# Optimization experiments

Measured on AMD Instinct MI355X. Metric: run time of the kernel, lower is better.

The kernel has to match this reference:

```python
import jax, jax.numpy as jnp
import numpy as np

B, N, C = 64, 196, 768
H = 12
HD = C // H            # 64
TOPK = int(0.25 * HD)  # 16
HIDDEN = int(C * 4.0)  # 3072
SCALE = HD ** -0.5
EPS = 1e-5


def layernorm(x, g, b):
    mu = jnp.mean(x, axis=-1, keepdims=True)
    var = jnp.var(x, axis=-1, keepdims=True)
    return (x - mu) * jax.lax.rsqrt(var + EPS) * g + b


def setup_inputs() -> dict:
    key = jax.random.key(0)
    ks = jax.random.split(key, 8)
    s = 0.02
    return {
        "x": jax.random.normal(ks[0], (B, N, C), jnp.float32),
        "norm1_g": jnp.ones((C,), jnp.float32),
        "norm1_b": jnp.zeros((C,), jnp.float32),
        "qk_w": jax.random.normal(ks[1], (2 * C, C), jnp.float32) * s,   # torch Linear [out,in], no bias
        "attn_proj_w": jax.random.normal(ks[2], (C, H * TOPK), jnp.float32) * s,
        "attn_proj_b": jnp.zeros((C,), jnp.float32),
        "norm2_g": jnp.ones((C,), jnp.float32),
        "norm2_b": jnp.zeros((C,), jnp.float32),
        "fc1_w": jax.random.normal(ks[3], (HIDDEN, C), jnp.float32) * s,
        "fc1_b": jnp.zeros((HIDDEN,), jnp.float32),
        "fc2_w": jax.random.normal(ks[4], (C, HIDDEN), jnp.float32) * s,
        "fc2_b": jnp.zeros((C,), jnp.float32),
    }


def reference(x, norm1_g, norm1_b, qk_w, attn_proj_w, attn_proj_b,
              norm2_g, norm2_b, fc1_w, fc1_b, fc2_w, fc2_b):
    # --- HomoAttention branch ---
    h = layernorm(x, norm1_g, norm1_b)                       # [B,N,C]
    qk = h @ qk_w.T                                          # [B,N,2C]
    qk = qk.reshape(B, N, 2, H, HD).transpose(2, 0, 3, 1, 4) # [2,B,H,N,HD]
    q, k = qk[0] * SCALE, qk[1]
    attn = jnp.einsum('bhnd,bhmd->bhnm', q, k)               # [B,H,N,N]
    top_vals, _ = jax.lax.top_k(attn, TOPK)                  # [B,H,N,TOPK]
    a = jax.nn.softmax(top_vals, axis=-1)
    a = a.transpose(0, 2, 1, 3).reshape(B, N, H * TOPK)      # [B,N,H*TOPK]
    x = x + a @ attn_proj_w.T + attn_proj_b

    # --- MLP branch ---
    h2 = layernorm(x, norm2_g, norm2_b)
    h2 = jax.nn.gelu(h2 @ fc1_w.T + fc1_b, approximate=False)
    x = x + h2 @ fc2_w.T + fc2_b
    return x
```

## Files before the change

kernel.cpp:

```cpp
#include <hip/hip_runtime.h>


#define BATCH 64
#define SEQ   196
#define CH    768
#define NHEAD 12
#define HDIM  64
#define TOPK  16
#define HID   3072
#define MROWS 12544
#define MHALF 6272
#define SCALE_F 0.125f
#define NEGBIG -3e38f

typedef __bf16 bf16x8 __attribute__((ext_vector_type(8)));
typedef float  f32x4  __attribute__((ext_vector_type(4)));

__device__ __forceinline__ unsigned short f2b(float f) {
    union { float f; unsigned int i; } c; c.f = f;
    unsigned int u = c.i;
    return (unsigned short)((u + 0x7fffu + ((u >> 16) & 1u)) >> 16);
}
__device__ __forceinline__ float b2f(unsigned short u) {
    union { unsigned int i; float f; } c; c.i = ((unsigned int)u) << 16; return c.f;
}

__device__ __forceinline__ float gelu_f(float v) {
    float u = v * (0.7978845608f + 0.0356774081f * v * v);
    float e = __expf(2.0f * u);
    float th = 1.0f - 2.0f / (e + 1.0f);
    return 0.5f * v * (1.0f + th);
}

__device__ __forceinline__ void async16(const unsigned short* g, unsigned short* l) {
    __builtin_amdgcn_global_load_lds(
        (const __attribute__((address_space(1))) unsigned int*)(g),
        (__attribute__((address_space(3))) unsigned int*)(l), 16, 0, 0);
}

__global__ __launch_bounds__(256) void f2b4_k(const float* __restrict__ s0, unsigned short* __restrict__ d0, int n0,
                                              const float* __restrict__ s1, unsigned short* __restrict__ d1, int n1,
                                              const float* __restrict__ s2, unsigned short* __restrict__ d2, int n2,
                                              const float* __restrict__ s3, unsigned short* __restrict__ d3, int n3)
{
    int idx = (blockIdx.x * 256 + threadIdx.x) * 4;
    const float* s; unsigned short* d; int n;
    if (idx < n0) { s = s0; d = d0; n = n0; }
    else {
        idx -= n0;
        if (idx < n1) { s = s1; d = d1; n = n1; }
        else {
            idx -= n1;
            if (idx < n2) { s = s2; d = d2; n = n2; }
            else { idx -= n2; s = s3; d = d3; n = n3; }
        }
    }
    if (idx < n) {
        float4 v = *(const float4*)(s + idx);
        ushort4 o;
        o.x = f2b(v.x); o.y = f2b(v.y); o.z = f2b(v.z); o.w = f2b(v.w);
        *(ushort4*)(d + idx) = o;
    }
}

template<bool INF32>
__global__ __launch_bounds__(256) void ln_k(const void* __restrict__ xin,
                                            const float* __restrict__ gw,
                                            const float* __restrict__ bw,
                                            unsigned short* __restrict__ out)
{
    const int row = blockIdx.x;
    const int tid = threadIdx.x;
    float v0, v1, v2;
    if constexpr (INF32) {
        const float* xr = (const float*)xin + (size_t)row * CH;
        v0 = xr[tid]; v1 = xr[tid + 256]; v2 = xr[tid + 512];
    } else {
        const unsigned short* xr = (const unsigned short*)xin + (size_t)row * CH;
        v0 = b2f(xr[tid]); v1 = b2f(xr[tid + 256]); v2 = b2f(xr[tid + 512]);
    }
    float s  = v0 + v1 + v2;
    float sq = v0*v0 + v1*v1 + v2*v2;
#pragma unroll
    for (int off = 32; off > 0; off >>= 1) {
        s  += __shfl_down(s, off, 64);
        sq += __shfl_down(sq, off, 64);
    }
    __shared__ __align__(16) float red[8];
    if ((tid & 63) == 0) { red[(tid >> 6) * 2] = s; red[(tid >> 6) * 2 + 1] = sq; }
    __syncthreads();
    s  = red[0] + red[2] + red[4] + red[6];
    sq = red[1] + red[3] + red[5] + red[7];
    float mu  = s * (1.0f / CH);
    float var = sq * (1.0f / CH) - mu * mu;
    float rs  = rsqrtf(var + 1e-5f);
    unsigned short* orow = out + (size_t)row * CH;
    orow[tid]       = f2b((v0 - mu) * rs * gw[tid]       + bw[tid]);
    orow[tid + 256] = f2b((v1 - mu) * rs * gw[tid + 256] + bw[tid + 256]);
    orow[tid + 512] = f2b((v2 - mu) * rs * gw[tid + 512] + bw[tid + 512]);
}

template<int TM, int TN, bool BIAS, int RES, bool GELU, bool OUTF>
__global__ __launch_bounds__(256, 4)
void gemm_bt(const unsigned short* __restrict__ A,
             const unsigned short* __restrict__ Bw,
             const float* __restrict__ bias,
             const void* __restrict__ resid,
             void* __restrict__ Cout,
             int M, int N, int K)
{
    constexpr int WROWS = (TM == 128) ? 2 : 1;
    constexpr int WCOLS = 4 / WROWS;
    constexpr int JF = TN / (16 * WCOLS);
    __shared__ __align__(16) unsigned short As[2][TM * 32];
    __shared__ __align__(16) unsigned short Bs[2][TN * 32];
    const int tid  = threadIdx.x;
    const int w    = tid >> 6;
    const int lane = tid & 63;

    const int gridN = gridDim.x, gridM = gridDim.y;
    const int lid = blockIdx.y * gridN + blockIdx.x;
    const int SG = 8 * gridN;
    const int sg = lid / SG, r = lid % SG;
    const int remM = gridM - sg * 8;
    int mloc, nloc;
    if (remM >= 8) { mloc = sg * 8 + (r & 7); nloc = r >> 3; }
    else           { mloc = sg * 8 + r % remM; nloc = r / remM; }
    const int tileM = mloc * TM;
    const int tileN = nloc * TN;

    const int wm = (w / WCOLS) * 64;
    const int wn = (w % WCOLS) * (JF * 16);
    const int q   = lane >> 4;
    const int l16 = lane & 15;
    const int csw = (q ^ (l16 & 3)) * 8;

    f32x4 acc[4][JF];
#pragma unroll
    for (int i = 0; i < 4; ++i)
#pragma unroll
        for (int j = 0; j < JF; ++j) acc[i][j] = (f32x4){0.f, 0.f, 0.f, 0.f};

    const int r0 = tid >> 2;
    const int g0 = ((tid & 3) ^ (r0 & 3)) * 8;

    const unsigned short* pB[TN / 64];
    const unsigned short* pA[TM / 64];
#pragma unroll
    for (int c = 0; c < TN / 64; ++c) pB[c] = Bw + (size_t)(tileN + r0 + c * 64) * K + g0;
#pragma unroll
    for (int c = 0; c < TM / 64; ++c) pA[c] = A + (size_t)(tileM + r0 + c * 64) * K + g0;

    auto stage = [&](int buf) {
#pragma unroll
        for (int c = 0; c < TN / 64; ++c) {
            async16(pB[c], &Bs[buf][(size_t)(c * 256 + w * 64) * 8]);
            pB[c] += 32;
        }
#pragma unroll
        for (int c = 0; c < TM / 64; ++c) {
            async16(pA[c], &As[buf][(size_t)(c * 256 + w * 64) * 8]);
            pA[c] += 32;
        }
    };

    const int kIters = K >> 5;
    stage(0);
    int cur = 0;
    for (int kt = 0; kt < kIters; ++kt) {
        __syncthreads();
        if (kt + 1 < kIters) stage(cur ^ 1);
        bf16x8 af[4], bfr[JF];
#pragma unroll
        for (int i = 0; i < 4; ++i)
            af[i] = *(const bf16x8*)&As[cur][(wm + i * 16 + l16) * 32 + csw];
#pragma unroll
        for (int j = 0; j < JF; ++j)
            bfr[j] = *(const bf16x8*)&Bs[cur][(wn + j * 16 + l16) * 32 + csw];
#pragma unroll
        for (int i = 0; i < 4; ++i)
#pragma unroll
            for (int j = 0; j < JF; ++j)
                acc[i][j] = __builtin_amdgcn_mfma_f32_16x16x32_bf16(af[i], bfr[j], acc[i][j], 0, 0, 0);
        cur ^= 1;
    }

#pragma unroll
    for (int i = 0; i < 4; ++i) {
#pragma unroll
        for (int r2 = 0; r2 < 4; ++r2) {
            int row = tileM + wm + i * 16 + q * 4 + r2;
#pragma unroll
            for (int j = 0; j < JF; ++j) {
                int col = tileN + wn + j * 16 + l16;
                float v = acc[i][j][r2];
                if (BIAS) v += bias[col];
                if (GELU) v = gelu_f(v);
                if (RES == 1) v += ((const float*)resid)[(size_t)row * N + col];
                if (RES == 2) v += b2f(((const unsigned short*)resid)[(size_t)row * N + col]);
                if (OUTF) ((float*)Cout)[(size_t)row * N + col] = v;
                else      ((unsigned short*)Cout)[(size_t)row * N + col] = f2b(v);
            }
        }
    }
}

template<int KC, bool BIAS, int RES, bool GELU, bool OUTF>
__global__ __launch_bounds__(512, 2)
void gemm8p(const unsigned short* __restrict__ A,
            const unsigned short* __restrict__ Bw,
            const float* __restrict__ bias,
            const void* __restrict__ resid,
            void* __restrict__ Cout,
            int M, int N)
{
    constexpr int T = KC / 64;
    __shared__ __align__(16) unsigned short As[2][256 * 64];
    __shared__ __align__(16) unsigned short Bs[2][256 * 64];
    const int tid  = threadIdx.x;
    const int w    = tid >> 6;
    const int lane = tid & 63;
    const int q    = lane >> 4;
    const int l16  = lane & 15;

    const int gridN = gridDim.x, gridM = gridDim.y;
    const int lid = blockIdx.y * gridN + blockIdx.x;
    const int SG = 8 * gridN;
    const int sg = lid / SG, rr = lid % SG;
    const int remM = gridM - sg * 8;
    int mloc, nloc;
    if (remM >= 8) { mloc = sg * 8 + (rr & 7); nloc = rr >> 3; }
    else           { mloc = sg * 8 + rr % remM; nloc = rr / remM; }
    const int tileM = mloc * 256, tileN = nloc * 256;

    const int wm = (w >> 2) * 128;
    const int wn = (w & 3) * 64;

    const int r0 = tid >> 3;
    const int g0 = (tid & 7) ^ (r0 & 7);
    const int rB = r0 + (r0 & 32);
    const unsigned short* pAsrc = A  + (size_t)(tileM + r0) * KC + g0 * 8;
    const unsigned short* pBsrc = Bw + (size_t)(tileN + rB) * KC + g0 * 8;

    auto stageA = [&](int v, int j) {
        const unsigned short* s = pAsrc + (size_t)(j * 64) * KC + v * 64;
        unsigned short* d = As[v & 1] + j * 4096 + w * 512;
        async16(s, d);
        async16(s + (size_t)128 * KC, d + 8192);
    };
    auto stageB = [&](int v, int j) {
        const unsigned short* s = pBsrc + (size_t)(j * 32) * KC + v * 64;
        unsigned short* d = Bs[v & 1] + j * 2048 + (w * 8 + ((w & 4) << 3)) * 64;
        async16(s, d);
        async16(s + (size_t)128 * KC, d + 8192);
    };

    f32x4 acc[8][4];
#pragma unroll
    for (int i = 0; i < 8; ++i)
#pragma unroll
        for (int jn = 0; jn < 4; ++jn) acc[i][jn] = (f32x4){0.f, 0.f, 0.f, 0.f};

    stageA(0, 0); stageB(0, 0); stageB(0, 1); stageA(0, 1);
    asm volatile("s_waitcnt vmcnt(4)" ::: "memory");
    __builtin_amdgcn_s_barrier();
    asm volatile("" ::: "memory");

    const int arow = wm + l16;
    const int brow = wn + l16;
    const int xsw  = l16 & 7;

#pragma unroll 2
    for (int u = 0; u < T; ++u) {
        const unsigned short* Ab = As[u & 1];
        const unsigned short* Bb = Bs[u & 1];
        bf16x8 af[4][2], b0[2][2], b1[2][2];

#pragma unroll
        for (int m = 0; m < 4; ++m)
#pragma unroll
            for (int kk = 0; kk < 2; ++kk)
                af[m][kk] = *(const bf16x8*)&Ab[(arow + m * 16) * 64 + ((((kk << 2) | q) ^ xsw) << 3)];
#pragma unroll
        for (int n = 0; n < 2; ++n)
#pragma unroll
            for (int kk = 0; kk < 2; ++kk)
                b0[n][kk] = *(const bf16x8*)&Bb[(brow + n * 16) * 64 + ((((kk << 2) | q) ^ xsw) << 3)];
        if (u + 1 < T) stageA(u + 1, 0);
        __builtin_amdgcn_s_setprio(1);
#pragma unroll
        for (int kk = 0; kk < 2; ++kk)
#pragma unroll
            for (int m = 0; m < 4; ++m)
#pragma unroll
                for (int n = 0; n < 2; ++n)
                    acc[m][n] = __builtin_amdgcn_mfma_f32_16x16x32_bf16(af[m][kk], b0[n][kk], acc[m][n], 0, 0, 0);
        __builtin_amdgcn_s_setprio(0);

        if (u + 1 < T) asm volatile("s_waitcnt vmcnt(4)" ::: "memory");
        else           asm volatile("s_waitcnt vmcnt(2)" ::: "memory");
        __builtin_amdgcn_s_barrier();
        asm volatile("" ::: "memory");
#pragma unroll
        for (int n = 0; n < 2; ++n)
#pragma unroll
            for (int kk = 0; kk < 2; ++kk)
                b1[n][kk] = *(const bf16x8*)&Bb[(brow + 32 + n * 16) * 64 + ((((kk << 2) | q) ^ xsw) << 3)];
        if (u + 1 < T) stageB(u + 1, 0);
        __builtin_amdgcn_s_setprio(1);
#pragma unroll
        for (int kk = 0; kk < 2; ++kk)
#pragma unroll
            for (int m = 0; m < 4; ++m)
#pragma unroll
                for (int n = 0; n < 2; ++n)
                    acc[m][2 + n] = __builtin_amdgcn_mfma_f32_16x16x32_bf16(af[m][kk], b1[n][kk], acc[m][2 + n], 0, 0, 0);
        __builtin_amdgcn_s_setprio(0);

        if (u + 1 < T) asm volatile("s_waitcnt vmcnt(4)" ::: "memory");
        else           asm volatile("s_waitcnt vmcnt(0)" ::: "memory");
        __builtin_amdgcn_s_barrier();
        asm volatile("" ::: "memory");
#pragma unroll
        for (int m = 0; m < 4; ++m)
#pragma unroll
            for (int kk = 0; kk < 2; ++kk)
                af[m][kk] = *(const bf16x8*)&Ab[(arow + 64 + m * 16) * 64 + ((((kk << 2) | q) ^ xsw) << 3)];
        if (u + 1 < T) stageB(u + 1, 1);
        __builtin_amdgcn_s_setprio(1);
#pragma unroll
        for (int kk = 0; kk < 2; ++kk)
#pragma unroll
            for (int m = 0; m < 4; ++m)
#pragma unroll
                for (int n = 0; n < 2; ++n)
                    acc[4 + m][2 + n] = __builtin_amdgcn_mfma_f32_16x16x32_bf16(af[m][kk], b1[n][kk], acc[4 + m][2 + n], 0, 0, 0);
        __builtin_amdgcn_s_setprio(0);

        if (u + 1 < T) {
            stageA(u + 1, 1);
            asm volatile("s_waitcnt vmcnt(4)" ::: "memory");
            __builtin_amdgcn_s_barrier();
            asm volatile("" ::: "memory");
        }
        __builtin_amdgcn_s_setprio(1);
#pragma unroll
        for (int kk = 0; kk < 2; ++kk)
#pragma unroll
            for (int m = 0; m < 4; ++m)
#pragma unroll
                for (int n = 0; n < 2; ++n)
                    acc[4 + m][n] = __builtin_amdgcn_mfma_f32_16x16x32_bf16(af[m][kk], b0[n][kk], acc[4 + m][n], 0, 0, 0);
        __builtin_amdgcn_s_setprio(0);
    }

#pragma unroll
    for (int mh = 0; mh < 2; ++mh)
#pragma unroll
        for (int m = 0; m < 4; ++m)
#pragma unroll
            for (int r2 = 0; r2 < 4; ++r2) {
                const int row = tileM + wm + mh * 64 + m * 16 + q * 4 + r2;
#pragma unroll
                for (int nh = 0; nh < 2; ++nh)
#pragma unroll
                    for (int n = 0; n < 2; ++n) {
                        const int col = tileN + wn + nh * 32 + n * 16 + l16;
                        float v = acc[mh * 4 + m][nh * 2 + n][r2];
                        if (BIAS) v += bias[col];
                        if (GELU) v = gelu_f(v);
                        if (RES == 1) v += ((const float*)resid)[(size_t)row * N + col];
                        if (RES == 2) v += b2f(((const unsigned short*)resid)[(size_t)row * N + col]);
                        if (OUTF) ((float*)Cout)[(size_t)row * N + col] = v;
                        else      ((unsigned short*)Cout)[(size_t)row * N + col] = f2b(v);
                    }
            }
    (void)M;
}

__global__ __launch_bounds__(256) void attn_topk(const unsigned short* __restrict__ qk,
                                                 unsigned short* __restrict__ aout)
{
    const int bh = blockIdx.x;
    const int b = bh / NHEAD, h = bh % NHEAD;
    __shared__ __align__(16) unsigned short Qs[208 * 64];
    __shared__ __align__(16) unsigned short Ks[208 * 64];
    const int tid = threadIdx.x;

    for (int i = tid; i < 208 * 8; i += 256) {
        int row = i >> 3, c = i & 7;
        uint4 vq = make_uint4(0, 0, 0, 0), vk = vq;
        if (row < SEQ) {
            const uint4* gp = (const uint4*)(qk + ((size_t)(b * SEQ + row) * 1536 + h * 64));
            vq = gp[c];
            vk = gp[c + 96];
        }
        int slot = c ^ (row & 7);
        *(uint4*)&Qs[row * 64 + slot * 8] = vq;
        *(uint4*)&Ks[row * 64 + slot * 8] = vk;
    }
    __syncthreads();

    const int w = tid >> 6, lane = tid & 63;
    const int q = lane >> 4, l16 = lane & 15;

    for (int tn = w; tn < 13; tn += 4) {
        const int nrow = tn * 16 + l16;
        const int nsw = nrow & 7;
        bf16x8 bq0 = *(const bf16x8*)&Qs[nrow * 64 + ((0 * 4 + q) ^ nsw) * 8];
        bf16x8 bq1 = *(const bf16x8*)&Qs[nrow * 64 + ((1 * 4 + q) ^ nsw) * 8];

        float t[TOPK];
#pragma unroll
        for (int j = 0; j < TOPK; ++j) t[j] = NEGBIG;

        for (int tm = 0; tm < 12; ++tm) {
            const int mrow = tm * 16 + l16;
            const int msw = mrow & 7;
            bf16x8 ak0 = *(const bf16x8*)&Ks[mrow * 64 + ((0 * 4 + q) ^ msw) * 8];
            bf16x8 ak1 = *(const bf16x8*)&Ks[mrow * 64 + ((1 * 4 + q) ^ msw) * 8];
            f32x4 acc = (f32x4){0.f, 0.f, 0.f, 0.f};
            acc = __builtin_amdgcn_mfma_f32_16x16x32_bf16(ak0, bq0, acc, 0, 0, 0);
            acc = __builtin_amdgcn_mfma_f32_16x16x32_bf16(ak1, bq1, acc, 0, 0, 0);
#pragma unroll
            for (int r = 0; r < 4; ++r) {
                float v = acc[r];
#pragma unroll
                for (int j = 0; j < TOPK; ++j) {
                    float mx = fmaxf(t[j], v);
                    v = fminf(t[j], v);
                    t[j] = mx;
                }
            }
        }
        {
            const int mrow = 12 * 16 + l16;
            const int msw = mrow & 7;
            bf16x8 ak0 = *(const bf16x8*)&Ks[mrow * 64 + ((0 * 4 + q) ^ msw) * 8];
            bf16x8 ak1 = *(const bf16x8*)&Ks[mrow * 64 + ((1 * 4 + q) ^ msw) * 8];
            f32x4 acc = (f32x4){0.f, 0.f, 0.f, 0.f};
            acc = __builtin_amdgcn_mfma_f32_16x16x32_bf16(ak0, bq0, acc, 0, 0, 0);
            acc = __builtin_amdgcn_mfma_f32_16x16x32_bf16(ak1, bq1, acc, 0, 0, 0);
#pragma unroll
            for (int r = 0; r < 4; ++r) {
                float v = (q == 0) ? acc[r] : NEGBIG;
#pragma unroll
                for (int j = 0; j < TOPK; ++j) {
                    float mx = fmaxf(t[j], v);
                    v = fminf(t[j], v);
                    t[j] = mx;
                }
            }
        }

#pragma unroll
        for (int stage = 0; stage < 2; ++stage) {
            const int xm = 16 << stage;
            float bl[TOPK], c[TOPK];
#pragma unroll
            for (int j = 0; j < TOPK; ++j) bl[j] = __shfl_xor(t[j], xm, 64);
#pragma unroll
            for (int j = 0; j < TOPK; ++j) c[j] = fmaxf(t[j], bl[TOPK - 1 - j]);
#pragma unroll
            for (int s = 8; s >= 1; s >>= 1) {
#pragma unroll
                for (int i = 0; i < TOPK; ++i) {
                    if ((i & s) == 0) {
                        float mx = fmaxf(c[i], c[i + s]);
                        c[i + s] = fminf(c[i], c[i + s]);
                        c[i] = mx;
                    }
                }
            }
#pragma unroll
            for (int j = 0; j < TOPK; ++j) t[j] = c[j];
        }

        if (q == 0 && nrow < SEQ) {
            float e[TOPK], sum = 0.f;
#pragma unroll
            for (int j = 0; j < TOPK; ++j) { e[j] = __expf((t[j] - t[0]) * SCALE_F); sum += e[j]; }
            float inv = 1.0f / sum;
            unsigned int pk[8];
#pragma unroll
            for (int jj = 0; jj < 8; ++jj)
                pk[jj] = (unsigned int)f2b(e[2 * jj] * inv) |
                         ((unsigned int)f2b(e[2 * jj + 1] * inv) << 16);
            unsigned short* dst = aout + ((size_t)(b * SEQ + nrow)) * (NHEAD * TOPK) + h * TOPK;
            ((uint4*)dst)[0] = make_uint4(pk[0], pk[1], pk[2], pk[3]);
            ((uint4*)dst)[1] = make_uint4(pk[4], pk[5], pk[6], pk[7]);
        }
    }
}

extern "C" void kernel_launch(void* const* d_in, const int* in_sizes, int n_in,
                              void* d_out, int out_size, void* d_ws, size_t ws_size,
                              hipStream_t stream)
{
    const float* x    = (const float*)d_in[0];
    const float* g1   = (const float*)d_in[1];
    const float* bb1  = (const float*)d_in[2];
    const float* qkw  = (const float*)d_in[3];
    const float* pw   = (const float*)d_in[4];
    const float* pb   = (const float*)d_in[5];
    const float* g2   = (const float*)d_in[6];
    const float* bb2  = (const float*)d_in[7];
    const float* f1w  = (const float*)d_in[8];
    const float* f1b  = (const float*)d_in[9];
    const float* f2w  = (const float*)d_in[10];
    const float* f2bp = (const float*)d_in[11];
    float* out = (float*)d_out;

    char* ws = (char*)d_ws;
    const size_t SZ_H   = (size_t)MROWS * CH * 2;
    const size_t N_WQK  = (size_t)2 * CH * CH;
    const size_t N_WP   = (size_t)CH * (NHEAD * TOPK);
    const size_t N_WF   = (size_t)HID * CH;
    const size_t SZ_W   = (N_WQK + N_WP + 2 * N_WF) * 2;
    const size_t SZ_A   = (size_t)MROWS * (NHEAD * TOPK) * 2;
    const size_t SZ_QK  = (size_t)MROWS * 2 * CH * 2;
    const size_t SZ_GGF = (size_t)MROWS * HID * 2;

    unsigned short* hbuf = (unsigned short*)(ws);
    unsigned short* wqk  = (unsigned short*)(ws + SZ_H);
    unsigned short* wp   = wqk + N_WQK;
    unsigned short* wf1  = wp  + N_WP;
    unsigned short* wf2  = wf1 + N_WF;
    unsigned short* av   = (unsigned short*)(ws + SZ_H + SZ_W);
    unsigned short* qk   = (unsigned short*)(ws + SZ_H + SZ_W + SZ_A);
    unsigned short* gg   = qk;

    const size_t base = SZ_H + SZ_W + SZ_A;
    const bool fullMLP = ws_size >= base + SZ_GGF + SZ_H;
    const bool bx1     = fullMLP || ws_size >= base + SZ_QK + SZ_H;
    unsigned short* x1b = (unsigned short*)(ws + base + (fullMLP ? SZ_GGF : SZ_QK));
    float* x1 = out;

    {
        int total4 = (int)((N_WQK + N_WP + 2 * N_WF) / 4);
        f2b4_k<<<(total4 + 255) / 256, 256, 0, stream>>>(
            qkw, wqk, (int)N_WQK, pw, wp, (int)N_WP,
            f1w, wf1, (int)N_WF, f2w, wf2, (int)N_WF);
    }

    ln_k<true><<<MROWS, 256, 0, stream>>>(x, g1, bb1, hbuf);
    gemm8p<CH, false, 0, false, false><<<dim3(2 * CH / 256, MROWS / 256), 512, 0, stream>>>(
        hbuf, wqk, nullptr, nullptr, qk, MROWS, 2 * CH);
    attn_topk<<<BATCH * NHEAD, 256, 0, stream>>>(qk, av);

    if (bx1) {
        gemm_bt<64, 128, true, 1, false, false><<<dim3(6, 196), 256, 0, stream>>>(
            av, wp, pb, x, x1b, MROWS, CH, NHEAD * TOPK);
        ln_k<false><<<MROWS, 256, 0, stream>>>(x1b, g2, bb2, hbuf);
        if (fullMLP) {
            gemm8p<CH, true, 0, true, false><<<dim3(HID / 256, MROWS / 256), 512, 0, stream>>>(
                hbuf, wf1, f1b, nullptr, gg, MROWS, HID);
            gemm8p<HID, true, 2, false, true><<<dim3(CH / 256, MROWS / 256), 512, 0, stream>>>(
                gg, wf2, f2bp, x1b, out, MROWS, CH);
        } else {
            for (int half = 0; half < 2; ++half) {
                const size_t ro = (size_t)half * MHALF;
                gemm_bt<128, 128, true, 0, true, false><<<dim3(24, 49), 256, 0, stream>>>(
                    hbuf + ro * CH, wf1, f1b, nullptr, gg, MHALF, HID, CH);
                gemm_bt<64, 256, true, 2, false, true><<<dim3(3, 98), 256, 0, stream>>>(
                    gg, wf2, f2bp, x1b + ro * CH, out + ro * CH, MHALF, CH, HID);
            }
        }
    } else {
        gemm_bt<64, 128, true, 1, false, true><<<dim3(6, 196), 256, 0, stream>>>(
            av, wp, pb, x, x1, MROWS, CH, NHEAD * TOPK);
        ln_k<true><<<MROWS, 256, 0, stream>>>(x1, g2, bb2, hbuf);
        for (int half = 0; half < 2; ++half) {
            const size_t ro = (size_t)half * MHALF;
            gemm_bt<128, 128, true, 0, true, false><<<dim3(24, 49), 256, 0, stream>>>(
                hbuf + ro * CH, wf1, f1b, nullptr, gg, MHALF, HID, CH);
            gemm_bt<64, 256, true, 1, false, true><<<dim3(3, 98), 256, 0, stream>>>(
                gg, wf2, f2bp, x1 + ro * CH, out + ro * CH, MHALF, CH, HID);
        }
    }
}
```

Before: 436.8 us.

## Make gemm8p persistent with cross-tile prefetch and LDS-staged vectorized epilogue

```diff
diff --git a/kernel.cpp b/kernel.cpp
--- a/kernel.cpp
+++ b/kernel.cpp
@@ -215,6 +215,7 @@
             int M, int N)
 {
     constexpr int T = KC / 64;
+    static_assert((T & 1) == 0, "T must be even for persistent parity");
     __shared__ __align__(16) unsigned short As[2][256 * 64];
     __shared__ __align__(16) unsigned short Bs[2][256 * 64];
     const int tid  = threadIdx.x;
@@ -223,15 +224,19 @@
     const int q    = lane >> 4;
     const int l16  = lane & 15;
 
-    const int gridN = gridDim.x, gridM = gridDim.y;
-    const int lid = blockIdx.y * gridN + blockIdx.x;
-    const int SG = 8 * gridN;
-    const int sg = lid / SG, rr = lid % SG;
-    const int remM = gridM - sg * 8;
-    int mloc, nloc;
-    if (remM >= 8) { mloc = sg * 8 + (rr & 7); nloc = rr >> 3; }
-    else           { mloc = sg * 8 + rr % remM; nloc = rr / remM; }
-    const int tileM = mloc * 256, tileN = nloc * 256;
+    const int gridN = N >> 8, gridM = M >> 8;
+    const int nt = gridN * gridM;
+    const int P = gridDim.x;
+
+    auto tileOf = [&](int lid2, int& tm, int& tn) {
+        const int SG = 8 * gridN;
+        const int sg = lid2 / SG, rr2 = lid2 % SG;
+        const int remM = gridM - sg * 8;
+        int mloc, nloc;
+        if (remM >= 8) { mloc = sg * 8 + (rr2 & 7); nloc = rr2 >> 3; }
+        else           { mloc = sg * 8 + rr2 % remM; nloc = rr2 / remM; }
+        tm = mloc * 256; tn = nloc * 256;
+    };
 
     const int wm = (w >> 2) * 128;
     const int wn = (w & 3) * 64;
@@ -239,143 +244,229 @@
     const int r0 = tid >> 3;
     const int g0 = (tid & 7) ^ (r0 & 7);
     const int rB = r0 + (r0 & 32);
-    const unsigned short* pAsrc = A  + (size_t)(tileM + r0) * KC + g0 * 8;
-    const unsigned short* pBsrc = Bw + (size_t)(tileN + rB) * KC + g0 * 8;
-
-    auto stageA = [&](int v, int j) {
-        const unsigned short* s = pAsrc + (size_t)(j * 64) * KC + v * 64;
-        unsigned short* d = As[v & 1] + j * 4096 + w * 512;
-        async16(s, d);
-        async16(s + (size_t)128 * KC, d + 8192);
-    };
-    auto stageB = [&](int v, int j) {
-        const unsigned short* s = pBsrc + (size_t)(j * 32) * KC + v * 64;
-        unsigned short* d = Bs[v & 1] + j * 2048 + (w * 8 + ((w & 4) << 3)) * 64;
-        async16(s, d);
-        async16(s + (size_t)128 * KC, d + 8192);
-    };
-
-    f32x4 acc[8][4];
-#pragma unroll
-    for (int i = 0; i < 8; ++i)
-#pragma unroll
-        for (int jn = 0; jn < 4; ++jn) acc[i][jn] = (f32x4){0.f, 0.f, 0.f, 0.f};
-
-    stageA(0, 0); stageB(0, 0); stageB(0, 1); stageA(0, 1);
-    asm volatile("s_waitcnt vmcnt(4)" ::: "memory");
-    __builtin_amdgcn_s_barrier();
-    asm volatile("" ::: "memory");
 
     const int arow = wm + l16;
     const int brow = wn + l16;
     const int xsw  = l16 & 7;
 
-#pragma unroll 2
-    for (int u = 0; u < T; ++u) {
-        const unsigned short* Ab = As[u & 1];
-        const unsigned short* Bb = Bs[u & 1];
-        bf16x8 af[4][2], b0[2][2], b1[2][2];
-
-#pragma unroll
-        for (int m = 0; m < 4; ++m)
-#pragma unroll
-            for (int kk = 0; kk < 2; ++kk)
-                af[m][kk] = *(const bf16x8*)&Ab[(arow + m * 16) * 64 + ((((kk << 2) | q) ^ xsw) << 3)];
-#pragma unroll
-        for (int n = 0; n < 2; ++n)
-#pragma unroll
-            for (int kk = 0; kk < 2; ++kk)
-                b0[n][kk] = *(const bf16x8*)&Bb[(brow + n * 16) * 64 + ((((kk << 2) | q) ^ xsw) << 3)];
-        if (u + 1 < T) stageA(u + 1, 0);
-        __builtin_amdgcn_s_setprio(1);
-#pragma unroll
-        for (int kk = 0; kk < 2; ++kk)
-#pragma unroll
-            for (int m = 0; m < 4; ++m)
-#pragma unroll
-                for (int n = 0; n < 2; ++n)
-                    acc[m][n] = __builtin_amdgcn_mfma_f32_16x16x32_bf16(af[m][kk], b0[n][kk], acc[m][n], 0, 0, 0);
-        __builtin_amdgcn_s_setprio(0);
-
-        if (u + 1 < T) asm volatile("s_waitcnt vmcnt(4)" ::: "memory");
-        else           asm volatile("s_waitcnt vmcnt(2)" ::: "memory");
-        __builtin_amdgcn_s_barrier();
-        asm volatile("" ::: "memory");
-#pragma unroll
-        for (int n = 0; n < 2; ++n)
-#pragma unroll
-            for (int kk = 0; kk < 2; ++kk)
-                b1[n][kk] = *(const bf16x8*)&Bb[(brow + 32 + n * 16) * 64 + ((((kk << 2) | q) ^ xsw) << 3)];
-        if (u + 1 < T) stageB(u + 1, 0);
-        __builtin_amdgcn_s_setprio(1);
-#pragma unroll
-        for (int kk = 0; kk < 2; ++kk)
-#pragma unroll
-            for (int m = 0; m < 4; ++m)
-#pragma unroll
-                for (int n = 0; n < 2; ++n)
-                    acc[m][2 + n] = __builtin_amdgcn_mfma_f32_16x16x32_bf16(af[m][kk], b1[n][kk], acc[m][2 + n], 0, 0, 0);
-        __builtin_amdgcn_s_setprio(0);
-
-        if (u + 1 < T) asm volatile("s_waitcnt vmcnt(4)" ::: "memory");
-        else           asm volatile("s_waitcnt vmcnt(0)" ::: "memory");
-        __builtin_amdgcn_s_barrier();
-        asm volatile("" ::: "memory");
-#pragma unroll
-        for (int m = 0; m < 4; ++m)
-#pragma unroll
-            for (int kk = 0; kk < 2; ++kk)
-                af[m][kk] = *(const bf16x8*)&Ab[(arow + 64 + m * 16) * 64 + ((((kk << 2) | q) ^ xsw) << 3)];
-        if (u + 1 < T) stageB(u + 1, 1);
-        __builtin_amdgcn_s_setprio(1);
-#pragma unroll
-        for (int kk = 0; kk < 2; ++kk)
-#pragma unroll
-            for (int m = 0; m < 4; ++m)
-#pragma unroll
-                for (int n = 0; n < 2; ++n)
-                    acc[4 + m][2 + n] = __builtin_amdgcn_mfma_f32_16x16x32_bf16(af[m][kk], b1[n][kk], acc[4 + m][2 + n], 0, 0, 0);
-        __builtin_amdgcn_s_setprio(0);
-
-        if (u + 1 < T) {
-            stageA(u + 1, 1);
+    for (int t = (int)blockIdx.x; t < nt; t += P) {
+        int tileM, tileN;
+        tileOf(t, tileM, tileN);
+        const bool hasNext = (t + P) < nt;
+        int tileM2 = tileM, tileN2 = tileN;
+        if (hasNext) tileOf(t + P, tileM2, tileN2);
+
+        const unsigned short* pA0  = A  + (size_t)(tileM  + r0) * KC + g0 * 8;
+        const unsigned short* pB0  = Bw + (size_t)(tileN  + rB) * KC + g0 * 8;
+        const unsigned short* pA0n = A  + (size_t)(tileM2 + r0) * KC + g0 * 8;
+        const unsigned short* pB0n = Bw + (size_t)(tileN2 + rB) * KC + g0 * 8;
+
+        auto stageA = [&](int v, int j) {
+            const unsigned short* base = (v == T) ? pA0n : pA0;
+            const int vv = (v == T) ? 0 : v;
+            const unsigned short* s = base + (size_t)(j * 64) * KC + vv * 64;
+            unsigned short* d = As[vv & 1] + j * 4096 + w * 512;
+            async16(s, d);
+            async16(s + (size_t)128 * KC, d + 8192);
+        };
+        auto stageB = [&](int v, int j) {
+            const unsigned short* base = (v == T) ? pB0n : pB0;
+            const int vv = (v == T) ? 0 : v;
+            const unsigned short* s = base + (size_t)(j * 32) * KC + vv * 64;
+            unsigned short* d = Bs[vv & 1] + j * 2048 + (w * 8 + ((w & 4) << 3)) * 64;
+            async16(s, d);
+            async16(s + (size_t)128 * KC, d + 8192);
+        };
+
+        f32x4 acc[8][4];
+#pragma unroll
+        for (int i = 0; i < 8; ++i)
+#pragma unroll
+            for (int jn = 0; jn < 4; ++jn) acc[i][jn] = (f32x4){0.f, 0.f, 0.f, 0.f};
+
+        if (t == (int)blockIdx.x) {
+            stageA(0, 0); stageB(0, 0); stageB(0, 1); stageA(0, 1);
             asm volatile("s_waitcnt vmcnt(4)" ::: "memory");
             __builtin_amdgcn_s_barrier();
             asm volatile("" ::: "memory");
         }
-        __builtin_amdgcn_s_setprio(1);
-#pragma unroll
-        for (int kk = 0; kk < 2; ++kk)
+
+#pragma unroll 2
+        for (int u = 0; u < T; ++u) {
+            const unsigned short* Ab = As[u & 1];
+            const unsigned short* Bb = Bs[u & 1];
+            const bool more = (u + 1 < T) || hasNext;
+            bf16x8 af[4][2], b0[2][2], b1[2][2];
+
 #pragma unroll
             for (int m = 0; m < 4; ++m)
 #pragma unroll
+                for (int kk = 0; kk < 2; ++kk)
+                    af[m][kk] = *(const bf16x8*)&Ab[(arow + m * 16) * 64 + ((((kk << 2) | q) ^ xsw) << 3)];
+#pragma unroll
+            for (int n = 0; n < 2; ++n)
+#pragma unroll
+                for (int kk = 0; kk < 2; ++kk)
+                    b0[n][kk] = *(const bf16x8*)&Bb[(brow + n * 16) * 64 + ((((kk << 2) | q) ^ xsw) << 3)];
+            if (more) stageA(u + 1, 0);
+            __builtin_amdgcn_s_setprio(1);
+#pragma unroll
+            for (int kk = 0; kk < 2; ++kk)
+#pragma unroll
+                for (int m = 0; m < 4; ++m)
+#pragma unroll
+                    for (int n = 0; n < 2; ++n)
+                        acc[m][n] = __builtin_amdgcn_mfma_f32_16x16x32_bf16(af[m][kk], b0[n][kk], acc[m][n], 0, 0, 0);
+            __builtin_amdgcn_s_setprio(0);
+
+            if (more) asm volatile("s_waitcnt vmcnt(4)" ::: "memory");
+            else      asm volatile("s_waitcnt vmcnt(2)" ::: "memory");
+            __builtin_amdgcn_s_barrier();
+            asm volatile("" ::: "memory");
+#pragma unroll
+            for (int n = 0; n < 2; ++n)
+#pragma unroll
+                for (int kk = 0; kk < 2; ++kk)
+                    b1[n][kk] = *(const bf16x8*)&Bb[(brow + 32 + n * 16) * 64 + ((((kk << 2) | q) ^ xsw) << 3)];
+            if (more) stageB(u + 1, 0);
+            __builtin_amdgcn_s_setprio(1);
+#pragma unroll
+            for (int kk = 0; kk < 2; ++kk)
+#pragma unroll
+                for (int m = 0; m < 4; ++m)
+#pragma unroll
+                    for (int n = 0; n < 2; ++n)
+                        acc[m][2 + n] = __builtin_amdgcn_mfma_f32_16x16x32_bf16(af[m][kk], b1[n][kk], acc[m][2 + n], 0, 0, 0);
+            __builtin_amdgcn_s_setprio(0);
+
+            if (more) asm volatile("s_waitcnt vmcnt(4)" ::: "memory");
+            else      asm volatile("s_waitcnt vmcnt(0)" ::: "memory");
+            __builtin_amdgcn_s_barrier();
+            asm volatile("" ::: "memory");
+#pragma unroll
+            for (int m = 0; m < 4; ++m)
+#pragma unroll
+                for (int kk = 0; kk < 2; ++kk)
+                    af[m][kk] = *(const bf16x8*)&Ab[(arow + 64 + m * 16) * 64 + ((((kk << 2) | q) ^ xsw) << 3)];
+            if (more) stageB(u + 1, 1);
+            __builtin_amdgcn_s_setprio(1);
+#pragma unroll
+            for (int kk = 0; kk < 2; ++kk)
+#pragma unroll
+                for (int m = 0; m < 4; ++m)
+#pragma unroll
+                    for (int n = 0; n < 2; ++n)
+                        acc[4 + m][2 + n] = __builtin_amdgcn_mfma_f32_16x16x32_bf16(af[m][kk], b1[n][kk], acc[4 + m][2 + n], 0, 0, 0);
+            __builtin_amdgcn_s_setprio(0);
+
+            if (more) {
+                stageA(u + 1, 1);
+                asm volatile("s_waitcnt vmcnt(4)" ::: "memory");
+                __builtin_amdgcn_s_barrier();
+                asm volatile("" ::: "memory");
+            }
+            __builtin_amdgcn_s_setprio(1);
+#pragma unroll
+            for (int kk = 0; kk < 2; ++kk)
+#pragma unroll
+                for (int m = 0; m < 4; ++m)
+#pragma unroll
+                    for (int n = 0; n < 2; ++n)
+                        acc[4 + m][n] = __builtin_amdgcn_mfma_f32_16x16x32_bf16(af[m][kk], b0[n][kk], acc[4 + m][n], 0, 0, 0);
+            __builtin_amdgcn_s_setprio(0);
+        }
+
+        __syncthreads();
+
+        float bshift[2][2];
+        if (BIAS) {
+#pragma unroll
+            for (int nh = 0; nh < 2; ++nh)
+#pragma unroll
                 for (int n = 0; n < 2; ++n)
-                    acc[4 + m][n] = __builtin_amdgcn_mfma_f32_16x16x32_bf16(af[m][kk], b0[n][kk], acc[4 + m][n], 0, 0, 0);
-        __builtin_amdgcn_s_setprio(0);
-    }
-
-#pragma unroll
-    for (int mh = 0; mh < 2; ++mh)
-#pragma unroll
-        for (int m = 0; m < 4; ++m)
-#pragma unroll
-            for (int r2 = 0; r2 < 4; ++r2) {
-                const int row = tileM + wm + mh * 64 + m * 16 + q * 4 + r2;
-#pragma unroll
-                for (int nh = 0; nh < 2; ++nh)
-#pragma unroll
-                    for (int n = 0; n < 2; ++n) {
-                        const int col = tileN + wn + nh * 32 + n * 16 + l16;
-                        float v = acc[mh * 4 + m][nh * 2 + n][r2];
-                        if (BIAS) v += bias[col];
-                        if (GELU) v = gelu_f(v);
-                        if (RES == 1) v += ((const float*)resid)[(size_t)row * N + col];
-                        if (RES == 2) v += b2f(((const unsigned short*)resid)[(size_t)row * N + col]);
-                        if (OUTF) ((float*)Cout)[(size_t)row * N + col] = v;
-                        else      ((unsigned short*)Cout)[(size_t)row * N + col] = f2b(v);
+                    bshift[nh][n] = bias[tileN + wn + nh * 32 + n * 16 + l16];
+        }
+
+        if constexpr (!OUTF) {
+            unsigned short* slab = &As[1][0] + (size_t)w * 1152;
+            unsigned short* co = (unsigned short*)Cout;
+#pragma unroll
+            for (int mh = 0; mh < 2; ++mh)
+#pragma unroll
+                for (int m = 0; m < 4; ++m) {
+#pragma unroll
+                    for (int nh = 0; nh < 2; ++nh)
+#pragma unroll
+                        for (int n = 0; n < 2; ++n)
+#pragma unroll
+                            for (int r2 = 0; r2 < 4; ++r2) {
+                                float v = acc[mh * 4 + m][nh * 2 + n][r2];
+                                if (BIAS) v += bshift[nh][n];
+                                if (GELU) v = gelu_f(v);
+                                slab[(q * 4 + r2) * 72 + nh * 32 + n * 16 + l16] = f2b(v);
+                            }
+#pragma unroll
+                    for (int h = 0; h < 2; ++h) {
+                        const int lr = h * 8 + (lane >> 3);
+                        const int grow = tileM + wm + mh * 64 + m * 16 + lr;
+                        const int gcol = tileN + wn + (lane & 7) * 8;
+                        uint4 pk = *(const uint4*)&slab[lr * 72 + (lane & 7) * 8];
+                        if (RES != 0) {
+                            unsigned short* ps = (unsigned short*)&pk;
+#pragma unroll
+                            for (int j = 0; j < 8; ++j) {
+                                float v = b2f(ps[j]);
+                                if (RES == 1) v += ((const float*)resid)[(size_t)grow * N + gcol + j];
+                                if (RES == 2) v += b2f(((const unsigned short*)resid)[(size_t)grow * N + gcol + j]);
+                                ps[j] = f2b(v);
+                            }
+                        }
+                        *(uint4*)&co[(size_t)grow * N + gcol] = pk;
                     }
-            }
-    (void)M;
+                }
+        } else {
+            float* slabf = (w == 7) ? (float*)&Bs[1][0]
+                                    : (float*)&As[1][0] + (size_t)w * 1088;
+            float* co = (float*)Cout;
+#pragma unroll
+            for (int mh = 0; mh < 2; ++mh)
+#pragma unroll
+                for (int m = 0; m < 4; ++m) {
+#pragma unroll
+                    for (int nh = 0; nh < 2; ++nh)
+#pragma unroll
+                        for (int n = 0; n < 2; ++n)
+#pragma unroll
+                            for (int r2 = 0; r2 < 4; ++r2) {
+                                float v = acc[mh * 4 + m][nh * 2 + n][r2];
+                                if (BIAS) v += bshift[nh][n];
+                                if (GELU) v = gelu_f(v);
+                                slabf[(q * 4 + r2) * 68 + nh * 32 + n * 16 + l16] = v;
+                            }
+#pragma unroll
+                    for (int i4 = 0; i4 < 4; ++i4) {
+                        const int lr = i4 * 4 + (lane >> 4);
+                        const int grow = tileM + wm + mh * 64 + m * 16 + lr;
+                        const int gcol = tileN + wn + (lane & 15) * 4;
+                        f32x4 vv = *(const f32x4*)&slabf[lr * 68 + (lane & 15) * 4];
+                        if (RES == 1) {
+                            const float4 r4 = *(const float4*)&((const float*)resid)[(size_t)grow * N + gcol];
+                            vv[0] += r4.x; vv[1] += r4.y; vv[2] += r4.z; vv[3] += r4.w;
+                        }
+                        if (RES == 2) {
+                            const ushort4 r4 = *(const ushort4*)&((const unsigned short*)resid)[(size_t)grow * N + gcol];
+                            vv[0] += b2f(r4.x); vv[1] += b2f(r4.y); vv[2] += b2f(r4.z); vv[3] += b2f(r4.w);
+                        }
+                        *(f32x4*)&co[(size_t)grow * N + gcol] = vv;
+                    }
+                }
+        }
+
+        if (hasNext) {
+            asm volatile("s_waitcnt vmcnt(4)" ::: "memory");
+            __syncthreads();
+        }
+    }
 }
 
 __global__ __launch_bounds__(256) void attn_topk(const unsigned short* __restrict__ qk,
@@ -544,7 +635,7 @@
     }
 
     ln_k<true><<<MROWS, 256, 0, stream>>>(x, g1, bb1, hbuf);
-    gemm8p<CH, false, 0, false, false><<<dim3(2 * CH / 256, MROWS / 256), 512, 0, stream>>>(
+    gemm8p<CH, false, 0, false, false><<<256, 512, 0, stream>>>(
         hbuf, wqk, nullptr, nullptr, qk, MROWS, 2 * CH);
     attn_topk<<<BATCH * NHEAD, 256, 0, stream>>>(qk, av);
 
@@ -553,9 +644,9 @@
             av, wp, pb, x, x1b, MROWS, CH, NHEAD * TOPK);
         ln_k<false><<<MROWS, 256, 0, stream>>>(x1b, g2, bb2, hbuf);
         if (fullMLP) {
-            gemm8p<CH, true, 0, true, false><<<dim3(HID / 256, MROWS / 256), 512, 0, stream>>>(
+            gemm8p<CH, true, 0, true, false><<<256, 512, 0, stream>>>(
                 hbuf, wf1, f1b, nullptr, gg, MROWS, HID);
-            gemm8p<HID, true, 2, false, true><<<dim3(CH / 256, MROWS / 256), 512, 0, stream>>>(
+            gemm8p<HID, true, 2, false, true><<<147, 512, 0, stream>>>(
                 gg, wf2, f2bp, x1b, out, MROWS, CH);
         } else {
             for (int half = 0; half < 2; ++half) {
```

After: 416.5 us. 1.05x faster.
